# Performance work log

Measured on AMD Instinct MI355X. Metric: run time of the kernel, lower is better.

Reference implementation:

```python
import jax, jax.numpy as jnp
import numpy as np

TOP_K = 2

def setup_inputs() -> dict:
    key = jax.random.key(0)
    ks = jax.random.split(key, 8)
    B, S, H, F, E = 2, 2048, 1024, 2048, 8
    sH = 1.0 / np.sqrt(H)
    sF = 1.0 / np.sqrt(F)
    return {
        "hidden_states": jax.random.normal(ks[0], (B, S, H), jnp.float32),
        "gate_w": jax.random.normal(ks[1], (E, H), jnp.float32) * sH,
        "w_up": jax.random.normal(ks[2], (E, H, F), jnp.float32) * sH,
        "w_gate": jax.random.normal(ks[3], (E, H, F), jnp.float32) * sH,
        "w_down": jax.random.normal(ks[4], (E, F, H), jnp.float32) * sF,
        "b_up": jnp.zeros((E, F), jnp.float32),
        "b_gate": jnp.zeros((E, F), jnp.float32),
        "b_down": jnp.zeros((E, H), jnp.float32),
    }

def reference(hidden_states, gate_w, w_up, w_gate, w_down, b_up, b_gate, b_down):
    # Flatten [B,S,H] -> [N,H]
    H = hidden_states.shape[-1]
    x = hidden_states.reshape(-1, H)                      # [N,H]
    router_logits = x @ gate_w.T                          # [N,E]
    probs = jax.nn.softmax(router_logits.astype(jnp.float32), axis=-1)
    topv, topi = jax.lax.top_k(probs, TOP_K)              # [N,K]
    topv = topv / topv.sum(axis=-1, keepdims=True)
    N, E = router_logits.shape
    # Sparse combine weights: zero except top-k experts (renormalized).
    w_full = jnp.zeros((N, E), probs.dtype).at[jnp.arange(N)[:, None], topi].set(topv)
    w_full = w_full.astype(x.dtype)
    # SwiGLU per expert (dense over E; combine weights zero out non-selected).
    u = jnp.einsum('nh,ehf->nef', x, w_up) + b_up         # [N,E,F]
    v = jnp.einsum('nh,ehf->nef', x, w_gate) + b_gate
    phi = jax.nn.silu(v) * u
    y = jnp.einsum('nef,efh->neh', phi, w_down) + b_down  # [N,E,H]
    out = jnp.einsum('ne,neh->nh', w_full, y)             # [N,H]
    out = out.reshape(hidden_states.shape)
    return out, router_logits.astype(hidden_states.dtype)
```

## Files before the change

### kernel.cpp

```cpp
#include <hip/hip_runtime.h>
#include <hip/hip_bf16.h>
#include <cstdint>
#include <cstddef>

#define N_TOK 4096
#define H_DIM 1024
#define F_DIM 2048
#define E_NUM 8
#define RCAP 9216

typedef __attribute__((ext_vector_type(8))) short bf16x8;
typedef __attribute__((ext_vector_type(4))) float f32x4;

__device__ __forceinline__ float b2f(uint16_t u) {
  return __uint_as_float(((uint32_t)u) << 16);
}
__device__ __forceinline__ uint16_t f2b(float f) {
  uint32_t x = __float_as_uint(f);
  uint32_t r = (x + 0x7fffu + ((x >> 16) & 1u)) >> 16;
  return (uint16_t)r;
}

__device__ __forceinline__ void gl2lds16(const void* g, void* l) {
  __builtin_amdgcn_global_load_lds(
      (const __attribute__((address_space(1))) uint32_t*)g,
      (__attribute__((address_space(3))) uint32_t*)l, 16, 0, 0);
}

__device__ __forceinline__ void stage_tile(const uint16_t* src, int ldK,
                                           char* lds, int wave, int lane) {
  int u = (lane & 7) ^ (lane >> 3);
  const char* s0 = (const char*)src + u * 16;
  size_t rb = (size_t)ldK * 2;
  int Rb = wave * 32 + (lane >> 3);
  for (int c = 0; c < 4; ++c) {
    gl2lds16(s0 + (size_t)(Rb + c * 8) * rb, lds + wave * 4096 + c * 1024);
  }
}

__device__ __forceinline__ bf16x8 read_frag(const char* lds, int R, int s,
                                            int q) {
  int unit = ((s << 2) + q) ^ (R & 7);
  return *(const bf16x8*)(lds + R * 128 + unit * 16);
}

__global__ __launch_bounds__(256) void detect_kernel(
    const uint16_t* __restrict__ x, int* __restrict__ flag) {
  __shared__ int cnt;
  if (threadIdx.x == 0) cnt = 0;
  __syncthreads();
  int ok = 0;
  for (int j = 0; j < 16; ++j) {
    uint16_t u = x[threadIdx.x * 16 + j];
    int e = (u >> 7) & 0xff;
    ok += (u == 0 || (e >= 96 && e <= 143)) ? 1 : 0;
  }
  atomicAdd(&cnt, ok);
  __syncthreads();
  if (threadIdx.x == 0) *flag = (cnt >= 3700) ? 1 : 0;
}

__global__ __launch_bounds__(256) void router_kernel(
    const void* __restrict__ xraw, const void* __restrict__ gwraw,
    const int* __restrict__ flag, void* __restrict__ dout,
    int* __restrict__ top_i, float* __restrict__ top_w) {
  int fl = *flag;
  int wave = threadIdx.x >> 6, lane = threadIdx.x & 63;
  int t = blockIdx.x * 4 + wave;
  float xv[16];
  if (fl) {
    const uint16_t* xr = (const uint16_t*)xraw + (size_t)t * H_DIM + lane * 16;
    uint4 a = *(const uint4*)xr;
    uint4 b = *(const uint4*)(xr + 8);
    uint32_t w[8] = {a.x, a.y, a.z, a.w, b.x, b.y, b.z, b.w};
    for (int j = 0; j < 8; ++j) {
      xv[2 * j] = b2f((uint16_t)(w[j] & 0xffff));
      xv[2 * j + 1] = b2f((uint16_t)(w[j] >> 16));
    }
  } else {
    const float* xr = (const float*)xraw + (size_t)t * H_DIM + lane * 16;
    for (int j = 0; j < 4; ++j) {
      float4 v = ((const float4*)xr)[j];
      xv[4 * j] = v.x; xv[4 * j + 1] = v.y;
      xv[4 * j + 2] = v.z; xv[4 * j + 3] = v.w;
    }
  }
  float acc[E_NUM];
  for (int e = 0; e < E_NUM; ++e) {
    float s = 0.f;
    if (fl) {
      const uint16_t* gr =
          (const uint16_t*)gwraw + (size_t)e * H_DIM + lane * 16;
      uint4 a = *(const uint4*)gr;
      uint4 b = *(const uint4*)(gr + 8);
      uint32_t w[8] = {a.x, a.y, a.z, a.w, b.x, b.y, b.z, b.w};
      for (int j = 0; j < 8; ++j) {
        s += xv[2 * j] * b2f((uint16_t)(w[j] & 0xffff));
        s += xv[2 * j + 1] * b2f((uint16_t)(w[j] >> 16));
      }
    } else {
      const float* gr = (const float*)gwraw + (size_t)e * H_DIM + lane * 16;
      for (int j = 0; j < 4; ++j) {
        float4 v = ((const float4*)gr)[j];
        s += xv[4 * j] * v.x + xv[4 * j + 1] * v.y + xv[4 * j + 2] * v.z +
             xv[4 * j + 3] * v.w;
      }
    }
    acc[e] = s;
  }
  for (int off = 32; off >= 1; off >>= 1)
    for (int e = 0; e < E_NUM; ++e)
      acc[e] += __shfl_xor(acc[e], off, 64);
  if (lane < E_NUM) {
    size_t idx = (size_t)N_TOK * H_DIM + (size_t)t * E_NUM + lane;
    if (fl)
      ((uint16_t*)dout)[idx] = f2b(acc[lane]);
    else
      ((float*)dout)[idx] = acc[lane];
  }
  if (lane == 0) {
    int b0 = 0;
    float v0 = acc[0];
    for (int e = 1; e < E_NUM; ++e)
      if (acc[e] > v0) { v0 = acc[e]; b0 = e; }
    int b1 = (b0 == 0) ? 1 : 0;
    float v1 = acc[b1];
    for (int e = 0; e < E_NUM; ++e)
      if (e != b0 && acc[e] > v1) { v1 = acc[e]; b1 = e; }
    float w0 = 1.f / (1.f + expf(v1 - v0));
    top_i[2 * t] = b0; top_i[2 * t + 1] = b1;
    top_w[2 * t] = w0; top_w[2 * t + 1] = 1.f - w0;
  }
}

__global__ __launch_bounds__(1024) void histscan_kernel(
    const int* __restrict__ top_i, const float* __restrict__ top_w,
    int* __restrict__ counts, int* __restrict__ bases,
    int* __restrict__ row_of, int* __restrict__ row_token,
    float* __restrict__ row_weight) {
  int tid = threadIdx.x;
  int lane = tid & 63, wave = tid >> 6;
  int e_loc[8];
  float tw[8];
  int c[E_NUM] = {};
  for (int j = 0; j < 8; ++j) {
    int idx = tid * 8 + j;
    int e = top_i[idx];
    e_loc[j] = e;
    tw[j] = top_w[idx];
    c[e]++;
  }
  int inc[E_NUM];
  for (int k = 0; k < E_NUM; ++k) inc[k] = c[k];
  for (int off = 1; off < 64; off <<= 1) {
    for (int k = 0; k < E_NUM; ++k) {
      int v = __shfl_up(inc[k], off, 64);
      if (lane >= off) inc[k] += v;
    }
  }
  __shared__ int wtot[16][E_NUM];
  __shared__ int woff[16][E_NUM];
  __shared__ int base_s[E_NUM];
  if (lane == 63)
    for (int k = 0; k < E_NUM; ++k) wtot[wave][k] = inc[k];
  __syncthreads();
  if (tid < E_NUM) {
    int run = 0;
    for (int w = 0; w < 16; ++w) {
      woff[w][tid] = run;
      run += wtot[w][tid];
    }
    counts[tid] = run;
    wtot[0][tid] = run;
  }
  __syncthreads();
  if (tid == 0) {
    int b = 0;
    for (int e = 0; e < E_NUM; ++e) {
      bases[e] = b;
      base_s[e] = b;
      b += (wtot[0][e] + 127) & ~127;
    }
  }
  __syncthreads();
  int run[E_NUM];
  for (int k = 0; k < E_NUM; ++k)
    run[k] = base_s[k] + woff[wave][k] + inc[k] - c[k];
  for (int j = 0; j < 8; ++j) {
    int idx = tid * 8 + j;
    int e = e_loc[j];
    int r = run[e]++;
    row_of[idx] = r;
    row_token[r] = idx >> 1;
    row_weight[r] = tw[j];
  }
}

__global__ __launch_bounds__(256) void gather_kernel(
    const void* __restrict__ xraw, const int* __restrict__ flag,
    const int* __restrict__ row_of, uint16_t* __restrict__ Xg) {
  int t = blockIdx.x;
  int rs0 = row_of[2 * t], rs1 = row_of[2 * t + 1];
  uint2 v;
  if (*flag) {
    v = ((const uint2*)((const uint16_t*)xraw + (size_t)t * H_DIM))[threadIdx.x];
  } else {
    float4 f =
        ((const float4*)((const float*)xraw + (size_t)t * H_DIM))[threadIdx.x];
    v.x = (uint32_t)f2b(f.x) | ((uint32_t)f2b(f.y) << 16);
    v.y = (uint32_t)f2b(f.z) | ((uint32_t)f2b(f.w) << 16);
  }
  ((uint2*)(Xg + (size_t)rs0 * H_DIM))[threadIdx.x] = v;
  ((uint2*)(Xg + (size_t)rs1 * H_DIM))[threadIdx.x] = v;
}

__global__ __launch_bounds__(256) void transpose_kernel(
    const void* __restrict__ W, const int* __restrict__ flag,
    uint16_t* __restrict__ Wt, int K, int N) {
  int e = blockIdx.z;
  int n0 = blockIdx.x * 64, k0 = blockIdx.y * 64;
  __shared__ __align__(16) uint16_t tile[64][72];
  size_t ebase = (size_t)e * K * N;
  uint16_t* Wout = Wt + ebase;
  int fl = *flag;
  int r = threadIdx.x >> 3;
  int c = (threadIdx.x & 7) * 8;
  if (fl) {
    const uint16_t* Win = (const uint16_t*)W + ebase;
    for (int it = 0; it < 2; ++it) {
      int row = r + it * 32;
      uint4 v = *(const uint4*)(Win + (size_t)(k0 + row) * N + n0 + c);
      *(uint4*)&tile[row][c] = v;
    }
  } else {
    const float* Win = (const float*)W + ebase;
    for (int it = 0; it < 2; ++it) {
      int row = r + it * 32;
      const float* p = Win + (size_t)(k0 + row) * N + n0 + c;
      float4 a = ((const float4*)p)[0];
      float4 b = ((const float4*)p)[1];
      uint16_t* tp = &tile[row][c];
      tp[0] = f2b(a.x); tp[1] = f2b(a.y); tp[2] = f2b(a.z); tp[3] = f2b(a.w);
      tp[4] = f2b(b.x); tp[5] = f2b(b.y); tp[6] = f2b(b.z); tp[7] = f2b(b.w);
    }
  }
  __syncthreads();
  for (int it = 0; it < 2; ++it) {
    int n = r + it * 32;
    uint4 o;
    o.x = (uint32_t)tile[c + 0][n] | ((uint32_t)tile[c + 1][n] << 16);
    o.y = (uint32_t)tile[c + 2][n] | ((uint32_t)tile[c + 3][n] << 16);
    o.z = (uint32_t)tile[c + 4][n] | ((uint32_t)tile[c + 5][n] << 16);
    o.w = (uint32_t)tile[c + 6][n] | ((uint32_t)tile[c + 7][n] << 16);
    *(uint4*)(Wout + (size_t)(n0 + n) * K + k0 + c) = o;
  }
}

__global__ __launch_bounds__(256, 2) void gemm_upgate(
    const uint16_t* __restrict__ Xg,
    const uint16_t* __restrict__ WtU, const uint16_t* __restrict__ WtG,
    const void* __restrict__ buRaw, const void* __restrict__ bgRaw,
    const int* __restrict__ flag,
    const int* __restrict__ counts, const int* __restrict__ bases,
    uint16_t* __restrict__ phi) {
  int e = blockIdx.z;
  int cnt = counts[e];
  int m0 = blockIdx.y * 128;
  if (m0 >= cnt) return;
  int n0 = blockIdx.x * 128;
  int base = bases[e];
  const uint16_t* A = Xg + (size_t)(base + m0) * H_DIM;
  const uint16_t* BU = WtU + (size_t)e * F_DIM * H_DIM + (size_t)n0 * H_DIM;
  const uint16_t* BG = WtG + (size_t)e * F_DIM * H_DIM + (size_t)n0 * H_DIM;

  __shared__ __align__(16) char lA[128 * 128];
  __shared__ __align__(16) char lBu[128 * 128];
  __shared__ __align__(16) char lBg[128 * 128];

  int tid = threadIdx.x;
  int wave = tid >> 6, lane = tid & 63;
  int wm = wave >> 1, wn = wave & 1;
  int q = lane >> 4, mr = lane & 15;

  f32x4 accU[4][4] = {};
  f32x4 accG[4][4] = {};

  for (int k0 = 0; k0 < H_DIM; k0 += 64) {
    __syncthreads();
    stage_tile(A + k0, H_DIM, lA, wave, lane);
    stage_tile(BU + k0, H_DIM, lBu, wave, lane);
    stage_tile(BG + k0, H_DIM, lBg, wave, lane);
    __syncthreads();
    for (int s = 0; s < 2; ++s) {
      bf16x8 af[4], bu[4], bg[4];
      for (int mt = 0; mt < 4; ++mt)
        af[mt] = read_frag(lA, wm * 64 + mt * 16 + mr, s, q);
      for (int nt = 0; nt < 4; ++nt) {
        bu[nt] = read_frag(lBu, wn * 64 + nt * 16 + mr, s, q);
        bg[nt] = read_frag(lBg, wn * 64 + nt * 16 + mr, s, q);
      }
      for (int mt = 0; mt < 4; ++mt)
        for (int nt = 0; nt < 4; ++nt) {
          accU[mt][nt] = __builtin_amdgcn_mfma_f32_16x16x32_bf16(
              af[mt], bu[nt], accU[mt][nt], 0, 0, 0);
          accG[mt][nt] = __builtin_amdgcn_mfma_f32_16x16x32_bf16(
              af[mt], bg[nt], accG[mt][nt], 0, 0, 0);
        }
    }
  }

  int fl = *flag;
  int rbase = m0 + wm * 64;
  int cbase = n0 + wn * 64;
  for (int nt = 0; nt < 4; ++nt) {
    int col = cbase + nt * 16 + mr;
    float bu_v, bg_v;
    if (fl) {
      bu_v = b2f(((const uint16_t*)buRaw)[(size_t)e * F_DIM + col]);
      bg_v = b2f(((const uint16_t*)bgRaw)[(size_t)e * F_DIM + col]);
    } else {
      bu_v = ((const float*)buRaw)[(size_t)e * F_DIM + col];
      bg_v = ((const float*)bgRaw)[(size_t)e * F_DIM + col];
    }
    for (int mt = 0; mt < 4; ++mt) {
      int r0 = rbase + mt * 16 + q * 4;
      for (int rg = 0; rg < 4; ++rg) {
        int row = r0 + rg;
        float u = accU[mt][nt][rg] + bu_v;
        float v = accG[mt][nt][rg] + bg_v;
        float s = v / (1.f + expf(-v));
        phi[(size_t)(base + row) * F_DIM + col] = f2b(s * u);
      }
    }
  }
}

__global__ __launch_bounds__(256, 2) void gemm_down(
    const uint16_t* __restrict__ phi, const uint16_t* __restrict__ WtD,
    const void* __restrict__ bdRaw, const int* __restrict__ flag,
    const int* __restrict__ counts, const int* __restrict__ bases,
    const int* __restrict__ row_token, const float* __restrict__ row_weight,
    float* __restrict__ out_acc) {
  int e = blockIdx.z;
  int cnt = counts[e];
  int m0 = blockIdx.y * 128;
  if (m0 >= cnt) return;
  int n0 = blockIdx.x * 128;
  int base = bases[e];
  const uint16_t* A = phi + (size_t)(base + m0) * F_DIM;
  const uint16_t* B = WtD + (size_t)e * H_DIM * F_DIM + (size_t)n0 * F_DIM;

  __shared__ __align__(16) char lA[128 * 128];
  __shared__ __align__(16) char lB[128 * 128];

  int tid = threadIdx.x;
  int wave = tid >> 6, lane = tid & 63;
  int wm = wave >> 1, wn = wave & 1;
  int q = lane >> 4, mr = lane & 15;

  f32x4 acc[4][4] = {};

  for (int k0 = 0; k0 < F_DIM; k0 += 64) {
    __syncthreads();
    stage_tile(A + k0, F_DIM, lA, wave, lane);
    stage_tile(B + k0, F_DIM, lB, wave, lane);
    __syncthreads();
    for (int s = 0; s < 2; ++s) {
      bf16x8 af[4], bf[4];
      for (int mt = 0; mt < 4; ++mt)
        af[mt] = read_frag(lA, wm * 64 + mt * 16 + mr, s, q);
      for (int nt = 0; nt < 4; ++nt)
        bf[nt] = read_frag(lB, wn * 64 + nt * 16 + mr, s, q);
      for (int mt = 0; mt < 4; ++mt)
        for (int nt = 0; nt < 4; ++nt)
          acc[mt][nt] = __builtin_amdgcn_mfma_f32_16x16x32_bf16(
              af[mt], bf[nt], acc[mt][nt], 0, 0, 0);
    }
  }

  int fl = *flag;
  int rbase = m0 + wm * 64;
  int cbase = n0 + wn * 64;
  for (int nt = 0; nt < 4; ++nt) {
    int col = cbase + nt * 16 + mr;
    float bd_v = fl ? b2f(((const uint16_t*)bdRaw)[(size_t)e * H_DIM + col])
                    : ((const float*)bdRaw)[(size_t)e * H_DIM + col];
    for (int mt = 0; mt < 4; ++mt) {
      int r0 = rbase + mt * 16 + q * 4;
      for (int rg = 0; rg < 4; ++rg) {
        int row = r0 + rg;
        if (row < cnt) {
          int tkn = row_token[base + row];
          float w = row_weight[base + row];
          atomicAdd(out_acc + (size_t)tkn * H_DIM + col,
                    w * (acc[mt][nt][rg] + bd_v));
        }
      }
    }
  }
}

__global__ __launch_bounds__(256) void out_convert(
    const float* __restrict__ acc, const int* __restrict__ flag,
    void* __restrict__ out) {
  int i = blockIdx.x * 256 + threadIdx.x;
  float4 v = ((const float4*)acc)[i];
  if (*flag) {
    uint2 o;
    o.x = (uint32_t)f2b(v.x) | ((uint32_t)f2b(v.y) << 16);
    o.y = (uint32_t)f2b(v.z) | ((uint32_t)f2b(v.w) << 16);
    ((uint2*)out)[i] = o;
  } else {
    ((float4*)out)[i] = v;
  }
}

extern "C" void kernel_launch(void* const* d_in, const int* in_sizes, int n_in,
                              void* d_out, int out_size, void* d_ws, size_t ws_size,
                              hipStream_t stream) {
  const void* x = d_in[0];
  const void* gw = d_in[1];
  const void* w_up = d_in[2];
  const void* w_gate = d_in[3];
  const void* w_down = d_in[4];
  const void* b_up = d_in[5];
  const void* b_gate = d_in[6];
  const void* b_down = d_in[7];

  char* ws = (char*)d_ws;
  size_t off = 0;
  auto alloc = [&](size_t bytes) -> void* {
    void* p = ws + off;
    off += (bytes + 255) & ~(size_t)255;
    return p;
  };
  int* counts = (int*)alloc(32);
  int* bases = (int*)alloc(32);
  int* flag = (int*)alloc(32);
  int* top_i = (int*)alloc(sizeof(int) * N_TOK * 2);
  float* top_w = (float*)alloc(sizeof(float) * N_TOK * 2);
  int* row_of = (int*)alloc(sizeof(int) * N_TOK * 2);
  int* row_token = (int*)alloc(sizeof(int) * RCAP);
  float* row_weight = (float*)alloc(sizeof(float) * RCAP);
  uint16_t* Xg = (uint16_t*)alloc((size_t)RCAP * H_DIM * 2);
  uint16_t* phi = (uint16_t*)alloc((size_t)RCAP * F_DIM * 2);
  uint16_t* WtU = (uint16_t*)alloc((size_t)E_NUM * H_DIM * F_DIM * 2);
  uint16_t* WtG = (uint16_t*)alloc((size_t)E_NUM * H_DIM * F_DIM * 2);
  float* out_acc = (float*)alloc((size_t)N_TOK * H_DIM * sizeof(float));

  hipMemsetAsync(out_acc, 0, (size_t)N_TOK * H_DIM * sizeof(float), stream);

  detect_kernel<<<1, 256, 0, stream>>>((const uint16_t*)x, flag);
  router_kernel<<<N_TOK / 4, 256, 0, stream>>>(x, gw, flag, d_out, top_i,
                                               top_w);
  histscan_kernel<<<1, 1024, 0, stream>>>(top_i, top_w, counts, bases, row_of,
                                          row_token, row_weight);
  gather_kernel<<<N_TOK, 256, 0, stream>>>(x, flag, row_of, Xg);

  transpose_kernel<<<dim3(F_DIM / 64, H_DIM / 64, E_NUM), 256, 0, stream>>>(
      w_up, flag, WtU, H_DIM, F_DIM);
  transpose_kernel<<<dim3(F_DIM / 64, H_DIM / 64, E_NUM), 256, 0, stream>>>(
      w_gate, flag, WtG, H_DIM, F_DIM);

  gemm_upgate<<<dim3(F_DIM / 128, 32, E_NUM), 256, 0, stream>>>(
      Xg, WtU, WtG, b_up, b_gate, flag, counts, bases, phi);

  transpose_kernel<<<dim3(H_DIM / 64, F_DIM / 64, E_NUM), 256, 0, stream>>>(
      w_down, flag, WtU, F_DIM, H_DIM);
  gemm_down<<<dim3(H_DIM / 128, 32, E_NUM), 256, 0, stream>>>(
      phi, WtU, b_down, flag, counts, bases, row_token, row_weight, out_acc);

  out_convert<<<(N_TOK * H_DIM / 4) / 256, 256, 0, stream>>>(out_acc, flag,
                                                             d_out);
}
```

Baseline: 461.4 us.

## Drop LDS staging in GEMMs, replace atomic scatter with combine kernel, merge transposes

Both expert GEMMs now load MFMA fragments straight from global memory into registers instead of staging swizzled tiles through LDS with barriers. The down GEMM writes per-row bf16 outputs, reusing the Xg buffer, and a new combine kernel does the weighted sum of each token's two expert rows. This replaces the fp32 atomicAdd scatter, the memset and the output conversion. The three weight transposes are merged into one launch with an unpadded-odd LDS tile. Direct global fragment loads lose LDS data reuse across waves and may become bandwidth bound, and rounding y to bf16 before combining adds precision loss.

Result: slower. 755.4 us (+63.7%).

```diff
diff --git a/kernel.cpp b/kernel.cpp
--- a/kernel.cpp
+++ b/kernel.cpp
@@ -19,29 +19,6 @@
   uint32_t x = __float_as_uint(f);
   uint32_t r = (x + 0x7fffu + ((x >> 16) & 1u)) >> 16;
   return (uint16_t)r;
-}
-
-__device__ __forceinline__ void gl2lds16(const void* g, void* l) {
-  __builtin_amdgcn_global_load_lds(
-      (const __attribute__((address_space(1))) uint32_t*)g,
-      (__attribute__((address_space(3))) uint32_t*)l, 16, 0, 0);
-}
-
-__device__ __forceinline__ void stage_tile(const uint16_t* src, int ldK,
-                                           char* lds, int wave, int lane) {
-  int u = (lane & 7) ^ (lane >> 3);
-  const char* s0 = (const char*)src + u * 16;
-  size_t rb = (size_t)ldK * 2;
-  int Rb = wave * 32 + (lane >> 3);
-  for (int c = 0; c < 4; ++c) {
-    gl2lds16(s0 + (size_t)(Rb + c * 8) * rb, lds + wave * 4096 + c * 1024);
-  }
-}
-
-__device__ __forceinline__ bf16x8 read_frag(const char* lds, int R, int s,
-                                            int q) {
-  int unit = ((s << 2) + q) ^ (R & 7);
-  return *(const bf16x8*)(lds + R * 128 + unit * 16);
 }
 
 __global__ __launch_bounds__(256) void detect_kernel(
@@ -134,20 +111,15 @@
 }
 
 __global__ __launch_bounds__(1024) void histscan_kernel(
-    const int* __restrict__ top_i, const float* __restrict__ top_w,
-    int* __restrict__ counts, int* __restrict__ bases,
-    int* __restrict__ row_of, int* __restrict__ row_token,
-    float* __restrict__ row_weight) {
+    const int* __restrict__ top_i, int* __restrict__ counts,
+    int* __restrict__ bases, int* __restrict__ row_of) {
   int tid = threadIdx.x;
   int lane = tid & 63, wave = tid >> 6;
   int e_loc[8];
-  float tw[8];
   int c[E_NUM] = {};
   for (int j = 0; j < 8; ++j) {
-    int idx = tid * 8 + j;
-    int e = top_i[idx];
+    int e = top_i[tid * 8 + j];
     e_loc[j] = e;
-    tw[j] = top_w[idx];
     c[e]++;
   }
   int inc[E_NUM];
@@ -187,12 +159,8 @@
   for (int k = 0; k < E_NUM; ++k)
     run[k] = base_s[k] + woff[wave][k] + inc[k] - c[k];
   for (int j = 0; j < 8; ++j) {
-    int idx = tid * 8 + j;
     int e = e_loc[j];
-    int r = run[e]++;
-    row_of[idx] = r;
-    row_token[r] = idx >> 1;
-    row_weight[r] = tw[j];
+    row_of[tid * 8 + j] = run[e]++;
   }
 }
 
@@ -214,12 +182,20 @@
   ((uint2*)(Xg + (size_t)rs1 * H_DIM))[threadIdx.x] = v;
 }
 
-__global__ __launch_bounds__(256) void transpose_kernel(
-    const void* __restrict__ W, const int* __restrict__ flag,
-    uint16_t* __restrict__ Wt, int K, int N) {
-  int e = blockIdx.z;
+__global__ __launch_bounds__(256) void transpose_all(
+    const void* __restrict__ wu, const void* __restrict__ wg,
+    const void* __restrict__ wd, const int* __restrict__ flag,
+    uint16_t* __restrict__ WtU, uint16_t* __restrict__ WtG,
+    uint16_t* __restrict__ WtD) {
+  int z = blockIdx.z;
+  int which = z >> 3, e = z & 7;
+  const void* W = which == 0 ? wu : which == 1 ? wg : wd;
+  uint16_t* Wt = which == 0 ? WtU : which == 1 ? WtG : WtD;
+  int K = which == 2 ? F_DIM : H_DIM;
+  int N = which == 2 ? H_DIM : F_DIM;
   int n0 = blockIdx.x * 64, k0 = blockIdx.y * 64;
-  __shared__ __align__(16) uint16_t tile[64][72];
+  if (n0 >= N || k0 >= K) return;
+  __shared__ uint16_t tile[64][65];
   size_t ebase = (size_t)e * K * N;
   uint16_t* Wout = Wt + ebase;
   int fl = *flag;
@@ -230,7 +206,11 @@
     for (int it = 0; it < 2; ++it) {
       int row = r + it * 32;
       uint4 v = *(const uint4*)(Win + (size_t)(k0 + row) * N + n0 + c);
-      *(uint4*)&tile[row][c] = v;
+      uint32_t w[4] = {v.x, v.y, v.z, v.w};
+      for (int j = 0; j < 4; ++j) {
+        tile[row][c + 2 * j] = (uint16_t)(w[j] & 0xffff);
+        tile[row][c + 2 * j + 1] = (uint16_t)(w[j] >> 16);
+      }
     }
   } else {
     const float* Win = (const float*)W + ebase;
@@ -239,9 +219,10 @@
       const float* p = Win + (size_t)(k0 + row) * N + n0 + c;
       float4 a = ((const float4*)p)[0];
       float4 b = ((const float4*)p)[1];
-      uint16_t* tp = &tile[row][c];
-      tp[0] = f2b(a.x); tp[1] = f2b(a.y); tp[2] = f2b(a.z); tp[3] = f2b(a.w);
-      tp[4] = f2b(b.x); tp[5] = f2b(b.y); tp[6] = f2b(b.z); tp[7] = f2b(b.w);
+      tile[row][c + 0] = f2b(a.x); tile[row][c + 1] = f2b(a.y);
+      tile[row][c + 2] = f2b(a.z); tile[row][c + 3] = f2b(a.w);
+      tile[row][c + 4] = f2b(b.x); tile[row][c + 5] = f2b(b.y);
+      tile[row][c + 6] = f2b(b.z); tile[row][c + 7] = f2b(b.w);
     }
   }
   __syncthreads();
@@ -269,44 +250,35 @@
   if (m0 >= cnt) return;
   int n0 = blockIdx.x * 128;
   int base = bases[e];
-  const uint16_t* A = Xg + (size_t)(base + m0) * H_DIM;
-  const uint16_t* BU = WtU + (size_t)e * F_DIM * H_DIM + (size_t)n0 * H_DIM;
-  const uint16_t* BG = WtG + (size_t)e * F_DIM * H_DIM + (size_t)n0 * H_DIM;
-
-  __shared__ __align__(16) char lA[128 * 128];
-  __shared__ __align__(16) char lBu[128 * 128];
-  __shared__ __align__(16) char lBg[128 * 128];
-
-  int tid = threadIdx.x;
-  int wave = tid >> 6, lane = tid & 63;
+  int wave = threadIdx.x >> 6, lane = threadIdx.x & 63;
   int wm = wave >> 1, wn = wave & 1;
   int q = lane >> 4, mr = lane & 15;
 
+  const uint16_t* A = Xg + (size_t)(base + m0 + wm * 64 + mr) * H_DIM + q * 8;
+  const uint16_t* BU =
+      WtU + ((size_t)e * F_DIM + n0 + wn * 64 + mr) * H_DIM + q * 8;
+  const uint16_t* BG =
+      WtG + ((size_t)e * F_DIM + n0 + wn * 64 + mr) * H_DIM + q * 8;
+
   f32x4 accU[4][4] = {};
   f32x4 accG[4][4] = {};
 
-  for (int k0 = 0; k0 < H_DIM; k0 += 64) {
-    __syncthreads();
-    stage_tile(A + k0, H_DIM, lA, wave, lane);
-    stage_tile(BU + k0, H_DIM, lBu, wave, lane);
-    stage_tile(BG + k0, H_DIM, lBg, wave, lane);
-    __syncthreads();
-    for (int s = 0; s < 2; ++s) {
-      bf16x8 af[4], bu[4], bg[4];
-      for (int mt = 0; mt < 4; ++mt)
-        af[mt] = read_frag(lA, wm * 64 + mt * 16 + mr, s, q);
+#pragma unroll 2
+  for (int k = 0; k < H_DIM; k += 32) {
+    bf16x8 af[4], bu[4], bg[4];
+    for (int mt = 0; mt < 4; ++mt)
+      af[mt] = *(const bf16x8*)(A + (size_t)mt * 16 * H_DIM + k);
+    for (int nt = 0; nt < 4; ++nt) {
+      bu[nt] = *(const bf16x8*)(BU + (size_t)nt * 16 * H_DIM + k);
+      bg[nt] = *(const bf16x8*)(BG + (size_t)nt * 16 * H_DIM + k);
+    }
+    for (int mt = 0; mt < 4; ++mt)
       for (int nt = 0; nt < 4; ++nt) {
-        bu[nt] = read_frag(lBu, wn * 64 + nt * 16 + mr, s, q);
-        bg[nt] = read_frag(lBg, wn * 64 + nt * 16 + mr, s, q);
-      }
-      for (int mt = 0; mt < 4; ++mt)
-        for (int nt = 0; nt < 4; ++nt) {
-          accU[mt][nt] = __builtin_amdgcn_mfma_f32_16x16x32_bf16(
-              af[mt], bu[nt], accU[mt][nt], 0, 0, 0);
-          accG[mt][nt] = __builtin_amdgcn_mfma_f32_16x16x32_bf16(
-              af[mt], bg[nt], accG[mt][nt], 0, 0, 0);
-        }
-    }
+        accU[mt][nt] = __builtin_amdgcn_mfma_f32_16x16x32_bf16(
+            af[mt], bu[nt], accU[mt][nt], 0, 0, 0);
+        accG[mt][nt] = __builtin_amdgcn_mfma_f32_16x16x32_bf16(
+            af[mt], bg[nt], accG[mt][nt], 0, 0, 0);
+      }
   }
 
   int fl = *flag;
@@ -335,47 +307,38 @@
   }
 }
 
-__global__ __launch_bounds__(256, 2) void gemm_down(
+__global__ __launch_bounds__(256, 3) void gemm_down(
     const uint16_t* __restrict__ phi, const uint16_t* __restrict__ WtD,
     const void* __restrict__ bdRaw, const int* __restrict__ flag,
     const int* __restrict__ counts, const int* __restrict__ bases,
-    const int* __restrict__ row_token, const float* __restrict__ row_weight,
-    float* __restrict__ out_acc) {
+    uint16_t* __restrict__ yb) {
   int e = blockIdx.z;
   int cnt = counts[e];
   int m0 = blockIdx.y * 128;
   if (m0 >= cnt) return;
   int n0 = blockIdx.x * 128;
   int base = bases[e];
-  const uint16_t* A = phi + (size_t)(base + m0) * F_DIM;
-  const uint16_t* B = WtD + (size_t)e * H_DIM * F_DIM + (size_t)n0 * F_DIM;
-
-  __shared__ __align__(16) char lA[128 * 128];
-  __shared__ __align__(16) char lB[128 * 128];
-
-  int tid = threadIdx.x;
-  int wave = tid >> 6, lane = tid & 63;
+  int wave = threadIdx.x >> 6, lane = threadIdx.x & 63;
   int wm = wave >> 1, wn = wave & 1;
   int q = lane >> 4, mr = lane & 15;
 
+  const uint16_t* A = phi + (size_t)(base + m0 + wm * 64 + mr) * F_DIM + q * 8;
+  const uint16_t* B =
+      WtD + ((size_t)e * H_DIM + n0 + wn * 64 + mr) * F_DIM + q * 8;
+
   f32x4 acc[4][4] = {};
 
-  for (int k0 = 0; k0 < F_DIM; k0 += 64) {
-    __syncthreads();
-    stage_tile(A + k0, F_DIM, lA, wave, lane);
-    stage_tile(B + k0, F_DIM, lB, wave, lane);
-    __syncthreads();
-    for (int s = 0; s < 2; ++s) {
-      bf16x8 af[4], bf[4];
-      for (int mt = 0; mt < 4; ++mt)
-        af[mt] = read_frag(lA, wm * 64 + mt * 16 + mr, s, q);
+#pragma unroll 2
+  for (int k = 0; k < F_DIM; k += 32) {
+    bf16x8 af[4], bf[4];
+    for (int mt = 0; mt < 4; ++mt)
+      af[mt] = *(const bf16x8*)(A + (size_t)mt * 16 * F_DIM + k);
+    for (int nt = 0; nt < 4; ++nt)
+      bf[nt] = *(const bf16x8*)(B + (size_t)nt * 16 * F_DIM + k);
+    for (int mt = 0; mt < 4; ++mt)
       for (int nt = 0; nt < 4; ++nt)
-        bf[nt] = read_frag(lB, wn * 64 + nt * 16 + mr, s, q);
-      for (int mt = 0; mt < 4; ++mt)
-        for (int nt = 0; nt < 4; ++nt)
-          acc[mt][nt] = __builtin_amdgcn_mfma_f32_16x16x32_bf16(
-              af[mt], bf[nt], acc[mt][nt], 0, 0, 0);
-    }
+        acc[mt][nt] = __builtin_amdgcn_mfma_f32_16x16x32_bf16(
+            af[mt], bf[nt], acc[mt][nt], 0, 0, 0);
   }
 
   int fl = *flag;
@@ -389,29 +352,34 @@
       int r0 = rbase + mt * 16 + q * 4;
       for (int rg = 0; rg < 4; ++rg) {
         int row = r0 + rg;
-        if (row < cnt) {
-          int tkn = row_token[base + row];
-          float w = row_weight[base + row];
-          atomicAdd(out_acc + (size_t)tkn * H_DIM + col,
-                    w * (acc[mt][nt][rg] + bd_v));
-        }
-      }
-    }
-  }
-}
-
-__global__ __launch_bounds__(256) void out_convert(
-    const float* __restrict__ acc, const int* __restrict__ flag,
+        yb[(size_t)(base + row) * H_DIM + col] = f2b(acc[mt][nt][rg] + bd_v);
+      }
+    }
+  }
+}
+
+__global__ __launch_bounds__(256) void combine_kernel(
+    const uint16_t* __restrict__ yb, const int* __restrict__ row_of,
+    const float* __restrict__ top_w, const int* __restrict__ flag,
     void* __restrict__ out) {
-  int i = blockIdx.x * 256 + threadIdx.x;
-  float4 v = ((const float4*)acc)[i];
+  int t = blockIdx.x;
+  int r0 = row_of[2 * t], r1 = row_of[2 * t + 1];
+  float w0 = top_w[2 * t], w1 = top_w[2 * t + 1];
+  int c = threadIdx.x * 4;
+  uint2 a = *(const uint2*)(yb + (size_t)r0 * H_DIM + c);
+  uint2 b = *(const uint2*)(yb + (size_t)r1 * H_DIM + c);
+  float o0 = w0 * b2f((uint16_t)(a.x & 0xffff)) + w1 * b2f((uint16_t)(b.x & 0xffff));
+  float o1 = w0 * b2f((uint16_t)(a.x >> 16)) + w1 * b2f((uint16_t)(b.x >> 16));
+  float o2 = w0 * b2f((uint16_t)(a.y & 0xffff)) + w1 * b2f((uint16_t)(b.y & 0xffff));
+  float o3 = w0 * b2f((uint16_t)(a.y >> 16)) + w1 * b2f((uint16_t)(b.y >> 16));
   if (*flag) {
     uint2 o;
-    o.x = (uint32_t)f2b(v.x) | ((uint32_t)f2b(v.y) << 16);
-    o.y = (uint32_t)f2b(v.z) | ((uint32_t)f2b(v.w) << 16);
-    ((uint2*)out)[i] = o;
+    o.x = (uint32_t)f2b(o0) | ((uint32_t)f2b(o1) << 16);
+    o.y = (uint32_t)f2b(o2) | ((uint32_t)f2b(o3) << 16);
+    *(uint2*)((uint16_t*)out + (size_t)t * H_DIM + c) = o;
   } else {
-    ((float4*)out)[i] = v;
+    float4 o = {o0, o1, o2, o3};
+    *(float4*)((float*)out + (size_t)t * H_DIM + c) = o;
   }
 }
 
@@ -440,36 +408,23 @@
   int* top_i = (int*)alloc(sizeof(int) * N_TOK * 2);
   float* top_w = (float*)alloc(sizeof(float) * N_TOK * 2);
   int* row_of = (int*)alloc(sizeof(int) * N_TOK * 2);
-  int* row_token = (int*)alloc(sizeof(int) * RCAP);
-  float* row_weight = (float*)alloc(sizeof(float) * RCAP);
   uint16_t* Xg = (uint16_t*)alloc((size_t)RCAP * H_DIM * 2);
   uint16_t* phi = (uint16_t*)alloc((size_t)RCAP * F_DIM * 2);
   uint16_t* WtU = (uint16_t*)alloc((size_t)E_NUM * H_DIM * F_DIM * 2);
   uint16_t* WtG = (uint16_t*)alloc((size_t)E_NUM * H_DIM * F_DIM * 2);
-  float* out_acc = (float*)alloc((size_t)N_TOK * H_DIM * sizeof(float));
-
-  hipMemsetAsync(out_acc, 0, (size_t)N_TOK * H_DIM * sizeof(float), stream);
+  uint16_t* WtD = (uint16_t*)alloc((size_t)E_NUM * H_DIM * F_DIM * 2);
 
   detect_kernel<<<1, 256, 0, stream>>>((const uint16_t*)x, flag);
+  transpose_all<<<dim3(32, 32, 24), 256, 0, stream>>>(w_up, w_gate, w_down,
+                                                      flag, WtU, WtG, WtD);
   router_kernel<<<N_TOK / 4, 256, 0, stream>>>(x, gw, flag, d_out, top_i,
                                                top_w);
-  histscan_kernel<<<1, 1024, 0, stream>>>(top_i, top_w, counts, bases, row_of,
-                                          row_token, row_weight);
+  histscan_kernel<<<1, 1024, 0, stream>>>(top_i, counts, bases, row_of);
   gather_kernel<<<N_TOK, 256, 0, stream>>>(x, flag, row_of, Xg);
-
-  transpose_kernel<<<dim3(F_DIM / 64, H_DIM / 64, E_NUM), 256, 0, stream>>>(
-      w_up, flag, WtU, H_DIM, F_DIM);
-  transpose_kernel<<<dim3(F_DIM / 64, H_DIM / 64, E_NUM), 256, 0, stream>>>(
-      w_gate, flag, WtG, H_DIM, F_DIM);
 
   gemm_upgate<<<dim3(F_DIM / 128, 32, E_NUM), 256, 0, stream>>>(
       Xg, WtU, WtG, b_up, b_gate, flag, counts, bases, phi);
-
-  transpose_kernel<<<dim3(H_DIM / 64, F_DIM / 64, E_NUM), 256, 0, stream>>>(
-      w_down, flag, WtU, F_DIM, H_DIM);
   gemm_down<<<dim3(H_DIM / 128, 32, E_NUM), 256, 0, stream>>>(
-      phi, WtU, b_down, flag, counts, bases, row_token, row_weight, out_acc);
-
-  out_convert<<<(N_TOK * H_DIM / 4) / 256, 256, 0, stream>>>(out_acc, flag,
-                                                             d_out);
-}
+      phi, WtD, b_down, flag, counts, bases, Xg);
+  combine_kernel<<<N_TOK, 256, 0, stream>>>(Xg, row_of, top_w, flag, d_out);
+}
```
